# Kernel tuning notes

Hardware: AMD Instinct MI355X
Metric: run time of the kernel (lower is better)

Reference implementation:

```python
import jax, jax.numpy as jnp
import numpy as np

H = W = 512
NUM_RINGS = 256  # min(image_shape) // 2
B = 128

def _make_bins():
    # Mirrors the torch __init__: fftshift=True, rfft=False
    center = np.array([H // 2, W // 2], dtype=np.float32)
    ii, jj = np.meshgrid(np.arange(H), np.arange(W), indexing='ij')
    coords = np.stack([ii, jj], -1).astype(np.float32) - center
    r = np.sqrt((coords ** 2).sum(-1))
    bins = np.round(r).astype(np.int32).reshape(-1)          # [H*W]
    mask = (bins > 3) & (bins < NUM_RINGS)                   # valid_bins_mask
    return bins, mask

def setup_inputs() -> dict:
    key = jax.random.key(0)
    k1, k2 = jax.random.split(key)
    parts = jax.random.normal(k1, (B, H, W), dtype=jnp.float32)
    projs = jax.random.normal(k2, (B, H, W), dtype=jnp.float32)
    bins, mask = _make_bins()
    return {
        "parts": parts,
        "projs": projs,
        "distance_bins": jnp.asarray(bins),
        "valid_mask": jnp.asarray(mask),
        "num_segments": int(bins.max()) + 1,  # static python int (= 363)
    }

def reference(parts, projs, distance_bins, valid_mask, num_segments):
    b = parts.shape[0]
    noise = (parts - projs).reshape(b, -1)                    # [B, H*W]
    a = jnp.abs(noise)

    seg = lambda x: jax.ops.segment_sum(x, distance_bins, num_segments=num_segments)
    counts = seg(jnp.ones(distance_bins.shape, jnp.float32))  # [NS], same for all batch rows

    # scatter_std (unbiased=True) ** 2 -> per-bin variance, two-pass
    sum_a = jax.vmap(seg)(a)                                  # [B, NS]
    mean = sum_a / jnp.maximum(counts, 1.0)[None, :]
    dev = a - mean[:, distance_bins]                          # gather mean back to pixels
    ssq = jax.vmap(seg)(dev * dev)                            # [B, NS]
    radial_var = ssq / jnp.maximum(counts - 1.0, 1.0)[None, :]

    flat_var = radial_var[:, distance_bins]                   # gather-broadcast [B, H*W]
    exp_term = -0.5 * (noise * noise) / flat_var
    logprob = exp_term - jnp.log(2.0 * jnp.pi * flat_var)
    logprob = jnp.where(valid_mask[None, :], logprob, 0.0).sum(-1, keepdims=True)  # [B, 1]
    return logprob
```

## Files before the change

kernel.cpp:

```cpp
#include <hip/hip_runtime.h>

#define HW (512 * 512)
#define NBINS 256
#define NB 128
#define NTILES 64
#define TPX 4096


__global__ __launch_bounds__(256) void tilesort(const int* __restrict__ bins,
                                                int* __restrict__ perm,
                                                int* __restrict__ tileCount,
                                                int* __restrict__ counts) {
    __shared__ int hist[NBINS];
    __shared__ int sc[NBINS];
    __shared__ int cursor[NBINS];
    const int t = threadIdx.x;
    const int tile = blockIdx.x;
    const int trow = tile >> 3, tcol = tile & 7;
    hist[t] = 0;
    __syncthreads();

    int myBins[16];
    #pragma unroll
    for (int k = 0; k < 4; ++k) {
        int row = (t >> 4) + k * 16;
        int col4 = t & 15;
        int4 v = *(const int4*)&bins[(trow * 64 + row) * 512 + tcol * 64 + col4 * 4];
        int bb[4] = {v.x, v.y, v.z, v.w};
        #pragma unroll
        for (int m = 0; m < 4; ++m) {
            myBins[k * 4 + m] = bb[m];
            if (bb[m] > 3 && bb[m] < NBINS) atomicAdd(&hist[bb[m]], 1);
        }
    }
    __syncthreads();
    sc[t] = hist[t];
    __syncthreads();
    for (int off = 1; off < 256; off <<= 1) {
        int x = (t >= off) ? sc[t - off] : 0;
        __syncthreads();
        sc[t] += x;
        __syncthreads();
    }
    cursor[t] = sc[t] - hist[t];
    if (t == 255) tileCount[tile] = sc[255];
    if (hist[t]) atomicAdd(&counts[t], hist[t]);
    __syncthreads();

    #pragma unroll
    for (int k = 0; k < 4; ++k) {
        int row = (t >> 4) + k * 16;
        int col4 = t & 15;
        #pragma unroll
        for (int m = 0; m < 4; ++m) {
            int bn = myBins[k * 4 + m];
            if (bn > 3 && bn < NBINS) {
                int local = row * 64 + col4 * 4 + m;
                int pos = atomicAdd(&cursor[bn], 1);
                perm[tile * TPX + pos] = (bn << 12) | local;
            }
        }
    }
}

__global__ __launch_bounds__(256) void pass(const float* __restrict__ parts,
                                            const float* __restrict__ projs,
                                            const int* __restrict__ perm,
                                            const int* __restrict__ tileCount,
                                            float* __restrict__ S1,
                                            float* __restrict__ S2) {
    __shared__ float sP[TPX], sQ[TPX];
    __shared__ float h1[NBINS], h2[NBINS];
    const int t = threadIdx.x;
    const int tile = blockIdx.x;
    const int b = blockIdx.y;
    const int trow = tile >> 3, tcol = tile & 7;
    h1[t] = 0.f; h2[t] = 0.f;

    const float* __restrict__ P = parts + (size_t)b * HW;
    const float* __restrict__ Q = projs + (size_t)b * HW;

    #pragma unroll
    for (int k = 0; k < 4; ++k) {
        int row = (t >> 4) + k * 16;
        int col4 = t & 15;
        const float4 p = *(const float4*)&P[(trow * 64 + row) * 512 + tcol * 64 + col4 * 4];
        const float4 q = *(const float4*)&Q[(trow * 64 + row) * 512 + tcol * 64 + col4 * 4];
        int x = row & 31;
        int rb = row * 64;
        sP[rb + ((col4 * 4 + 0) ^ x)] = p.x;
        sP[rb + ((col4 * 4 + 1) ^ x)] = p.y;
        sP[rb + ((col4 * 4 + 2) ^ x)] = p.z;
        sP[rb + ((col4 * 4 + 3) ^ x)] = p.w;
        sQ[rb + ((col4 * 4 + 0) ^ x)] = q.x;
        sQ[rb + ((col4 * 4 + 1) ^ x)] = q.y;
        sQ[rb + ((col4 * 4 + 2) ^ x)] = q.z;
        sQ[rb + ((col4 * 4 + 3) ^ x)] = q.w;
    }
    __syncthreads();

    const int count = tileCount[tile];
    const int e0 = t * 16;
    float a1 = 0.f, a2 = 0.f;
    int curBin = -1;

    if (e0 < count) {
        const int4* pe = (const int4*)(perm + tile * TPX + e0);
        #pragma unroll
        for (int g = 0; g < 4; ++g) {
            int4 e4 = pe[g];
            int ee[4] = {e4.x, e4.y, e4.z, e4.w};
            #pragma unroll
            for (int k2 = 0; k2 < 4; ++k2) {
                int idx = e0 + g * 4 + k2;
                if (idx < count) {
                    int e = ee[k2];
                    int bn = e >> 12;
                    int local = e & 4095;
                    int slot = local ^ ((local >> 6) & 31);
                    float n = sP[slot] - sQ[slot];
                    if (bn != curBin) {
                        if (curBin >= 0) {
                            atomicAdd(&h1[curBin], a1);
                            atomicAdd(&h2[curBin], a2);
                        }
                        curBin = bn; a1 = 0.f; a2 = 0.f;
                    }
                    a1 += fabsf(n);
                    a2 += n * n;
                }
            }
        }
        if (curBin >= 0) {
            atomicAdd(&h1[curBin], a1);
            atomicAdd(&h2[curBin], a2);
        }
    }
    __syncthreads();
    if (h1[t] != 0.f) unsafeAtomicAdd(&S1[b * NBINS + t], h1[t]);
    if (h2[t] != 0.f) unsafeAtomicAdd(&S2[b * NBINS + t], h2[t]);
}

__global__ __launch_bounds__(256) void finalize(const float* __restrict__ S1,
                                                const float* __restrict__ S2,
                                                const int* __restrict__ counts,
                                                float* __restrict__ out) {
    const int b = blockIdx.x;
    const int t = threadIdx.x;
    float contrib = 0.f;
    if (t > 3) {
        float c = (float)counts[t];
        float s1 = S1[b * NBINS + t];
        float s2 = S2[b * NBINS + t];
        float mean = s1 / fmaxf(c, 1.f);
        float ssq = fmaxf(s2 - mean * s1, 0.f);
        float var = ssq / fmaxf(c - 1.f, 1.f);
        contrib = -0.5f * s2 / var - c * logf(6.283185307179586f * var);
    }
    #pragma unroll
    for (int off = 32; off > 0; off >>= 1) contrib += __shfl_down(contrib, off, 64);
    __shared__ float w[4];
    if ((t & 63) == 0) w[t >> 6] = contrib;
    __syncthreads();
    if (t == 0) out[b] = w[0] + w[1] + w[2] + w[3];
}

extern "C" void kernel_launch(void* const* d_in, const int* in_sizes, int n_in,
                              void* d_out, int out_size, void* d_ws, size_t ws_size,
                              hipStream_t stream) {
    const float* parts = (const float*)d_in[0];
    const float* projs = (const float*)d_in[1];
    const int* bins    = (const int*)d_in[2];
    float* out = (float*)d_out;

    char* ws = (char*)d_ws;
    int*   tileCount = (int*)(ws + 0);
    int*   counts    = (int*)(ws + 512);
    float* S1        = (float*)(ws + 4096);
    float* S2        = (float*)(ws + 135168);
    int*   perm      = (int*)(ws + 266240);

    hipMemsetAsync(d_ws, 0, 266240, stream);

    tilesort<<<NTILES, 256, 0, stream>>>(bins, perm, tileCount, counts);
    pass    <<<dim3(NTILES, NB), 256, 0, stream>>>(parts, projs, perm, tileCount, S1, S2);
    finalize<<<NB, 256, 0, stream>>>(S1, S2, counts, out);
}
```

Baseline: 304.1 us.

## Process several batch images per block with register-prefetched tiles

```diff
diff --git a/kernel.cpp b/kernel.cpp
--- a/kernel.cpp
+++ b/kernel.cpp
@@ -5,6 +5,7 @@
 #define NB 128
 #define NTILES 64
 #define TPX 4096
+#define GB 8
 
 
 __global__ __launch_bounds__(256) void tilesort(const int* __restrict__ bins,
@@ -55,90 +56,117 @@
         for (int m = 0; m < 4; ++m) {
             int bn = myBins[k * 4 + m];
             if (bn > 3 && bn < NBINS) {
-                int local = row * 64 + col4 * 4 + m;
+                int col = col4 * 4 + m;
+                int slot = row * 64 + (col ^ (row & 31));
                 int pos = atomicAdd(&cursor[bn], 1);
-                perm[tile * TPX + pos] = (bn << 12) | local;
+                perm[tile * TPX + pos] = (bn << 16) | slot;
             }
         }
     }
 }
 
-__global__ __launch_bounds__(256) void pass(const float* __restrict__ parts,
-                                            const float* __restrict__ projs,
-                                            const int* __restrict__ perm,
-                                            const int* __restrict__ tileCount,
-                                            float* __restrict__ S1,
-                                            float* __restrict__ S2) {
+__global__ __launch_bounds__(256, 4) void pass(const float* __restrict__ parts,
+                                               const float* __restrict__ projs,
+                                               const int* __restrict__ perm,
+                                               const int* __restrict__ tileCount,
+                                               float* __restrict__ S1,
+                                               float* __restrict__ S2) {
     __shared__ float sP[TPX], sQ[TPX];
     __shared__ float h1[NBINS], h2[NBINS];
     const int t = threadIdx.x;
     const int tile = blockIdx.x;
-    const int b = blockIdx.y;
+    const int bg = blockIdx.y * GB;
     const int trow = tile >> 3, tcol = tile & 7;
     h1[t] = 0.f; h2[t] = 0.f;
 
-    const float* __restrict__ P = parts + (size_t)b * HW;
-    const float* __restrict__ Q = projs + (size_t)b * HW;
-
-    #pragma unroll
-    for (int k = 0; k < 4; ++k) {
-        int row = (t >> 4) + k * 16;
-        int col4 = t & 15;
-        const float4 p = *(const float4*)&P[(trow * 64 + row) * 512 + tcol * 64 + col4 * 4];
-        const float4 q = *(const float4*)&Q[(trow * 64 + row) * 512 + tcol * 64 + col4 * 4];
-        int x = row & 31;
-        int rb = row * 64;
-        sP[rb + ((col4 * 4 + 0) ^ x)] = p.x;
-        sP[rb + ((col4 * 4 + 1) ^ x)] = p.y;
-        sP[rb + ((col4 * 4 + 2) ^ x)] = p.z;
-        sP[rb + ((col4 * 4 + 3) ^ x)] = p.w;
-        sQ[rb + ((col4 * 4 + 0) ^ x)] = q.x;
-        sQ[rb + ((col4 * 4 + 1) ^ x)] = q.y;
-        sQ[rb + ((col4 * 4 + 2) ^ x)] = q.z;
-        sQ[rb + ((col4 * 4 + 3) ^ x)] = q.w;
-    }
-    __syncthreads();
-
     const int count = tileCount[tile];
     const int e0 = t * 16;
-    float a1 = 0.f, a2 = 0.f;
-    int curBin = -1;
-
-    if (e0 < count) {
+    int e[16];
+    {
         const int4* pe = (const int4*)(perm + tile * TPX + e0);
         #pragma unroll
-        for (int g = 0; g < 4; ++g) {
-            int4 e4 = pe[g];
-            int ee[4] = {e4.x, e4.y, e4.z, e4.w};
+        for (int g4 = 0; g4 < 4; ++g4) {
+            int4 e4 = pe[g4];
+            e[g4 * 4 + 0] = (e0 + g4 * 4 + 0 < count) ? e4.x : -1;
+            e[g4 * 4 + 1] = (e0 + g4 * 4 + 1 < count) ? e4.y : -1;
+            e[g4 * 4 + 2] = (e0 + g4 * 4 + 2 < count) ? e4.z : -1;
+            e[g4 * 4 + 3] = (e0 + g4 * 4 + 3 < count) ? e4.w : -1;
+        }
+    }
+
+    const int row0 = t >> 4;
+    const int cb = (t & 15) * 4;
+    const int gbase = (trow * 64 + row0) * 512 + tcol * 64 + cb;
+
+    float4 Pr[4], Qr[4];
+    {
+        const float* Pb = parts + (size_t)bg * HW;
+        const float* Qb = projs + (size_t)bg * HW;
+        #pragma unroll
+        for (int k = 0; k < 4; ++k) {
+            Pr[k] = *(const float4*)(Pb + gbase + k * 16 * 512);
+            Qr[k] = *(const float4*)(Qb + gbase + k * 16 * 512);
+        }
+    }
+
+    for (int g = 0; g < GB; ++g) {
+        __syncthreads();
+        #pragma unroll
+        for (int k = 0; k < 4; ++k) {
+            int row = row0 + 16 * k;
+            int x = row & 31;
+            int rb = row * 64;
+            sP[rb + ((cb + 0) ^ x)] = Pr[k].x;
+            sP[rb + ((cb + 1) ^ x)] = Pr[k].y;
+            sP[rb + ((cb + 2) ^ x)] = Pr[k].z;
+            sP[rb + ((cb + 3) ^ x)] = Pr[k].w;
+            sQ[rb + ((cb + 0) ^ x)] = Qr[k].x;
+            sQ[rb + ((cb + 1) ^ x)] = Qr[k].y;
+            sQ[rb + ((cb + 2) ^ x)] = Qr[k].z;
+            sQ[rb + ((cb + 3) ^ x)] = Qr[k].w;
+        }
+        if (g + 1 < GB) {
+            const float* Pn = parts + (size_t)(bg + g + 1) * HW;
+            const float* Qn = projs + (size_t)(bg + g + 1) * HW;
             #pragma unroll
-            for (int k2 = 0; k2 < 4; ++k2) {
-                int idx = e0 + g * 4 + k2;
-                if (idx < count) {
-                    int e = ee[k2];
-                    int bn = e >> 12;
-                    int local = e & 4095;
-                    int slot = local ^ ((local >> 6) & 31);
-                    float n = sP[slot] - sQ[slot];
-                    if (bn != curBin) {
-                        if (curBin >= 0) {
-                            atomicAdd(&h1[curBin], a1);
-                            atomicAdd(&h2[curBin], a2);
-                        }
-                        curBin = bn; a1 = 0.f; a2 = 0.f;
+            for (int k = 0; k < 4; ++k) {
+                Pr[k] = *(const float4*)(Pn + gbase + k * 16 * 512);
+                Qr[k] = *(const float4*)(Qn + gbase + k * 16 * 512);
+            }
+        }
+        __syncthreads();
+
+        float a1 = 0.f, a2 = 0.f;
+        int curBin = -1;
+        #pragma unroll
+        for (int k = 0; k < 16; ++k) {
+            int bn = e[k] >> 16;
+            if (bn >= 0) {
+                int slot = e[k] & 0xFFF;
+                float n = sP[slot] - sQ[slot];
+                if (bn != curBin) {
+                    if (curBin >= 0) {
+                        unsafeAtomicAdd(&h1[curBin], a1);
+                        unsafeAtomicAdd(&h2[curBin], a2);
                     }
-                    a1 += fabsf(n);
-                    a2 += n * n;
+                    curBin = bn; a1 = 0.f; a2 = 0.f;
                 }
+                a1 += fabsf(n);
+                a2 += n * n;
             }
         }
         if (curBin >= 0) {
-            atomicAdd(&h1[curBin], a1);
-            atomicAdd(&h2[curBin], a2);
-        }
-    }
-    __syncthreads();
-    if (h1[t] != 0.f) unsafeAtomicAdd(&S1[b * NBINS + t], h1[t]);
-    if (h2[t] != 0.f) unsafeAtomicAdd(&S2[b * NBINS + t], h2[t]);
+            unsafeAtomicAdd(&h1[curBin], a1);
+            unsafeAtomicAdd(&h2[curBin], a2);
+        }
+        __syncthreads();
+
+        const int b = bg + g;
+        float v1 = h1[t], v2 = h2[t];
+        if (v1 != 0.f) unsafeAtomicAdd(&S1[b * NBINS + t], v1);
+        if (v2 != 0.f) unsafeAtomicAdd(&S2[b * NBINS + t], v2);
+        h1[t] = 0.f; h2[t] = 0.f;
+    }
 }
 
 __global__ __launch_bounds__(256) void finalize(const float* __restrict__ S1,
@@ -183,6 +211,6 @@
     hipMemsetAsync(d_ws, 0, 266240, stream);
 
     tilesort<<<NTILES, 256, 0, stream>>>(bins, perm, tileCount, counts);
-    pass    <<<dim3(NTILES, NB), 256, 0, stream>>>(parts, projs, perm, tileCount, S1, S2);
+    pass    <<<dim3(NTILES, NB / GB), 256, 0, stream>>>(parts, projs, perm, tileCount, S1, S2);
     finalize<<<NB, 256, 0, stream>>>(S1, S2, counts, out);
 }
```

Result: no change. 307.0 us (+0.9%).
